# Kernel optimization log

Hardware: AMD Instinct MI355X
Metric: run time of the kernel (lower is better)

The kernel has to match this reference:

```python
import jax, jax.numpy as jnp
import numpy as np

N = 100000   # nodes
E = 1600000  # edges
R = 5        # num relations = num_edge_types + 2
H = 64       # hidden_dim
K = 10000    # absorbed nodes (<= MAX_NODES PE table)
NT = 11      # num_node_types + 1
NB = 2       # num_bases


def setup_inputs() -> dict:
    key = jax.random.key(0)
    ks = jax.random.split(key, 20)
    x = jax.random.randint(ks[0], (N,), 0, NT, dtype=jnp.int32)
    edge_index = jax.random.randint(ks[1], (2, E), 0, N, dtype=jnp.int32)
    edge_type = jax.random.randint(ks[2], (E,), 0, R, dtype=jnp.int32)
    node_order = jnp.arange(K, dtype=jnp.int32)
    emb = jax.random.normal(ks[3], (NT, H), dtype=jnp.float32) * 0.1
    inp = {"x": x, "edge_index": edge_index, "edge_type": edge_type,
           "node_order": node_order, "emb": emb}
    dims = [(H, H), (H, H), (H, 1)]
    i = 4
    for l, (din, dout) in enumerate(dims):
        inp[f"bases{l}"] = jax.random.normal(ks[i], (NB, din, dout), dtype=jnp.float32) / np.sqrt(din); i += 1
        inp[f"comp{l}"] = jax.random.normal(ks[i], (R, NB), dtype=jnp.float32) * 0.5; i += 1
        inp[f"root{l}"] = jax.random.normal(ks[i], (din, dout), dtype=jnp.float32) / np.sqrt(din); i += 1
        inp[f"bias{l}"] = jnp.zeros((dout,), dtype=jnp.float32)
    return inp


def rgcn_conv(h, src, dst, etype, bases, comp, root, bias):
    # Basis decomposition: W_r = sum_b comp[r,b] * bases[b]   -> [R, in, out]
    W = jnp.einsum('rb,bio->rio', comp, bases)
    # Transform every node by every relation weight (small R), then gather per edge.
    xW = jnp.einsum('ni,rio->nro', h, W)            # [N, R, out]
    msg = xW[src, etype]                            # [E, out]
    # Per-relation MEAN aggregation (PyG RGCNConv default): normalize each edge
    # by the count of edges with the same (dst, relation).
    seg = dst * R + etype                           # [E]
    cnt = jax.ops.segment_sum(jnp.ones((E,), h.dtype), seg, num_segments=N * R)
    norm = 1.0 / jnp.maximum(cnt[seg], 1.0)         # [E]
    agg = jax.ops.segment_sum(msg * norm[:, None], dst, num_segments=N)  # [N, out]
    return agg + h @ root + bias


def reference(x, edge_index, edge_type, node_order, emb,
              bases0, comp0, root0, bias0,
              bases1, comp1, root1, bias1,
              bases2, comp2, root2, bias2):
    h = emb[x]                                      # [N, H]
    # Positional encoding with out_channels=1: pe[t, 0] = sin((t+1) * 1.0),
    # broadcast-added across the hidden dim of each absorbed node.
    pe = jnp.sin(jnp.arange(1, K + 1, dtype=jnp.float32))[:, None]  # [K, 1]
    h = h.at[node_order].add(jnp.broadcast_to(pe, (K, H)))
    src, dst = edge_index[0], edge_index[1]
    h = rgcn_conv(h, src, dst, edge_type, bases0, comp0, root0, bias0)
    h = rgcn_conv(h, src, dst, edge_type, bases1, comp1, root1, bias1)
    h = rgcn_conv(h, src, dst, edge_type, bases2, comp2, root2, bias2)  # [N, 1]
    absorbed = jnp.zeros((N,), bool).at[node_order].set(True)
    unmasked = (~absorbed).astype(h.dtype)[:, None]  # [N, 1]
    eh = jnp.exp(h)
    denom = jnp.sum(eh * unmasked, axis=0)           # sum over unmasked rows
    return (eh / denom) * unmasked                   # absorbed rows zeroed
```

## Files before the change

kernel.cpp:

```cpp
#include <hip/hip_runtime.h>
#include <hip/hip_fp16.h>
#include <math.h>

#define NN 100000
#define NE 1600000
#define RR 5
#define HH 64
#define KK 10000
#define NBB 2
#define NBK 391
#define EPB 6250
#define BSLOT 4608
#define MPITCH 136

typedef _Float16 f16x8 __attribute__((ext_vector_type(8)));
typedef float f32x4 __attribute__((ext_vector_type(4)));

__global__ void k_init_h(const int* __restrict__ x, const float4* __restrict__ emb4,
                         unsigned short* __restrict__ hH, int* __restrict__ bcur,
                         int* __restrict__ absorbed, float* __restrict__ denom) {
    int idx = blockIdx.x * blockDim.x + threadIdx.x;
    if (idx >= NN * 16) return;
    int n = idx >> 4;
    int q = idx & 15;
    float4 v = emb4[x[n] * 16 + q];
    __half2 lo = __floats2half2_rn(v.x, v.y);
    __half2 hi = __floats2half2_rn(v.z, v.w);
    *(uint2*)&hH[(size_t)n * HH + q * 4] = make_uint2(*(unsigned*)&lo, *(unsigned*)&hi);
    if (idx < NBK) bcur[idx] = 0;
    if (idx == NBK) denom[0] = 0.f;
    if (idx < NN) absorbed[idx] = 0;
}

__global__ void k_pe(const int* __restrict__ order, unsigned short* __restrict__ hH,
                     int* __restrict__ absorbed) {
    int idx = blockIdx.x * blockDim.x + threadIdx.x;
    if (idx >= KK * 16) return;
    int t = idx >> 4;
    int q = idx & 15;
    int node = order[t];
    float v = (float)sin((double)(t + 1));
    uint2 u = *(uint2*)&hH[(size_t)node * HH + q * 4];
    float2 lo = __half22float2(*(__half2*)&u.x);
    float2 hi = __half22float2(*(__half2*)&u.y);
    __half2 nlo = __floats2half2_rn(lo.x + v, lo.y + v);
    __half2 nhi = __floats2half2_rn(hi.x + v, hi.y + v);
    *(uint2*)&hH[(size_t)node * HH + q * 4] = make_uint2(*(unsigned*)&nlo, *(unsigned*)&nhi);
    if (q == 0) absorbed[node] = 1;
}

__global__ void k_bplace(const int* __restrict__ src, const int* __restrict__ dst,
                         const int* __restrict__ et, int* __restrict__ bcur,
                         unsigned int* __restrict__ ebuf) {
    __shared__ int hist[NBK];
    __shared__ int lbase[NBK];
    __shared__ int lcur[NBK];
    int tid = threadIdx.x;
    for (int i = tid; i < NBK; i += 256) { hist[i] = 0; lcur[i] = 0; }
    __syncthreads();
    int e0 = blockIdx.x * EPB;
    int e1 = e0 + EPB < NE ? e0 + EPB : NE;
    for (int e = e0 + tid; e < e1; e += 256)
        atomicAdd(&hist[dst[e] >> 8], 1);
    __syncthreads();
    for (int i = tid; i < NBK; i += 256)
        if (hist[i]) lbase[i] = i * BSLOT + atomicAdd(&bcur[i], hist[i]);
    __syncthreads();
    for (int e = e0 + tid; e < e1; e += 256) {
        int d = dst[e];
        int b = d >> 8;
        int r = atomicAdd(&lcur[b], 1);
        int idx = lbase[b] + r;
        if (idx < (b + 1) * BSLOT)
            ebuf[idx] = ((unsigned)(d & 255) << 20) | ((unsigned)src[e] << 3) | (unsigned)et[e];
    }
}

__launch_bounds__(256)
__global__ void k_bsort(const unsigned int* __restrict__ ebuf, const int* __restrict__ bcur,
                        unsigned int* __restrict__ epair, int2* __restrict__ rowse,
                        float* __restrict__ norm5g) {
    __shared__ unsigned int el[BSLOT];
    __shared__ int cnt5[256 * RR];
    __shared__ int dcur[256];
    __shared__ int s[256];
    int tid = threadIdx.x;
    int b = blockIdx.x;
    int base = b * BSLOT;
    int sz = bcur[b];
    if (sz > BSLOT) sz = BSLOT;

    for (int i = tid; i < sz; i += 256) el[i] = ebuf[base + i];
    for (int i = tid; i < 256 * RR; i += 256) cnt5[i] = 0;
    __syncthreads();
    for (int i = tid; i < sz; i += 256) {
        unsigned int e = el[i];
        atomicAdd(&cnt5[(e >> 20) * RR + (e & 7)], 1);
    }
    __syncthreads();
    int deg = 0;
#pragma unroll
    for (int r = 0; r < RR; r++) deg += cnt5[tid * RR + r];
    s[tid] = deg;
    dcur[tid] = 0;
    __syncthreads();
#pragma unroll
    for (int off = 1; off < 256; off <<= 1) {
        int t = (tid >= off) ? s[tid - off] : 0;
        __syncthreads();
        s[tid] += t;
        __syncthreads();
    }
    int rs = s[tid] - deg;
    int d = b * 256 + tid;
    if (d < NN) {
        rowse[d] = make_int2(base + rs, base + rs + deg);
#pragma unroll
        for (int r = 0; r < RR; r++) {
            int c = cnt5[tid * RR + r];
            norm5g[(size_t)d * RR + r] = 1.0f / (float)(c > 1 ? c : 1);
        }
    }
    __syncthreads();
    for (int i = tid; i < sz; i += 256) {
        unsigned int e = el[i];
        int d8 = e >> 20;
        int rk = atomicAdd(&dcur[d8], 1);
        int pos = base + (s[d8] - (cnt5[d8 * RR + 0] + cnt5[d8 * RR + 1] + cnt5[d8 * RR + 2]
                                   + cnt5[d8 * RR + 3] + cnt5[d8 * RR + 4])) + rk;
        unsigned int cnt = (unsigned)cnt5[d8 * RR + (e & 7)];
        epair[pos] = (cnt << 23) | (e & 0xFFFFFu);
    }
}

__global__ void k_makeWt(const float* __restrict__ b0, const float* __restrict__ r0,
                         const float* __restrict__ b1, const float* __restrict__ r1,
                         unsigned short* __restrict__ Wt) {
    int idx = blockIdx.x * 256 + threadIdx.x;
    if (idx >= 2 * 64 * 192) return;
    int layer = idx / (64 * 192);
    int rem = idx - layer * 64 * 192;
    int o = rem / 192, k = rem - o * 192;
    const float* bases = layer ? b1 : b0;
    const float* root  = layer ? r1 : r0;
    float w = (k < 64)  ? bases[(size_t)k * HH + o]
            : (k < 128) ? bases[(size_t)HH * HH + (size_t)(k - 64) * HH + o]
                        : root[(size_t)(k - 128) * HH + o];
    __half hv = __float2half_rn(w);
    Wt[idx] = *(unsigned short*)&hv;
}

template <int DO2>
__launch_bounds__(256)
__global__ void k_layer(const int2* __restrict__ rowse, const unsigned int* __restrict__ epair,
                        const float* __restrict__ norm5g, const float* __restrict__ comp,
                        const unsigned short* __restrict__ hH, const unsigned short* __restrict__ Wt,
                        const float* __restrict__ bias, unsigned short* __restrict__ outH,
                        const float* __restrict__ bases2, const float* __restrict__ comp2,
                        const float* __restrict__ root2, const float* __restrict__ bias2,
                        float* __restrict__ xW2, float* __restrict__ h2) {
    __shared__ float2 lut[8];
    __shared__ float2 wlutS[64][8];
    __shared__ _Float16 mixs[64][MPITCH];
    __shared__ float sW2[6 * HH];
    int tid = threadIdx.x;
    int wave = tid >> 6;
    int lane = tid & 63;
    if (tid < 8) {
        int r = tid < RR ? tid : 0;
        lut[tid] = make_float2(comp[r * NBB + 0], comp[r * NBB + 1]);
    }
    if (DO2) {
        for (int i2 = tid; i2 < 6 * HH; i2 += 256) {
            int c = i2 >> 6, k = i2 & 63;
            sW2[i2] = (c < RR) ? (comp2[c * NBB + 0] * bases2[k] + comp2[c * NBB + 1] * bases2[HH + k])
                               : root2[k];
        }
    }
    __syncthreads();

    int n0 = blockIdx.x * 64;
    int g  = lane >> 3;
    int dq = lane & 7;

    for (int i = 0; i < 2; ++i) {
        int row = wave * 16 + i * 8 + g;
        int node = n0 + row;
        float m0[8] = {}, m1[8] = {};
        int beg = 0, end = 0;
        if (node < NN) { int2 se = rowse[node]; beg = se.x; end = se.y; }
        float nv = (dq < RR && node < NN) ? norm5g[(size_t)node * RR + dq] : 0.f;
        float2 cw = (dq < RR) ? make_float2(lut[dq].x * nv, lut[dq].y * nv)
                              : make_float2(0.f, 0.f);
        wlutS[row][dq] = cw;

        unsigned int p[8];
#pragma unroll
        for (int u = 0; u < 8; ++u) p[u] = (beg + u < end) ? epair[beg + u] : 5u;
        for (int j = beg; j < end; j += 8) {
            unsigned int q[8];
#pragma unroll
            for (int u = 0; u < 8; ++u)
                q[u] = (j + 8 + u < end) ? epair[j + 8 + u] : 5u;
            uint4 ua[8];
#pragma unroll
            for (int u = 0; u < 8; ++u)
                ua[u] = *(const uint4*)&hH[(size_t)((p[u] >> 3) & 0x1FFFFu) * HH + dq * 8];
#pragma unroll
            for (int u = 0; u < 8; ++u) {
                float2 cc = wlutS[row][p[u] & 7];
                float a0 = cc.x, a1 = cc.y;
                float2 f;
                f = __half22float2(*(__half2*)&ua[u].x);
                m0[0] += a0 * f.x; m0[1] += a0 * f.y; m1[0] += a1 * f.x; m1[1] += a1 * f.y;
                f = __half22float2(*(__half2*)&ua[u].y);
                m0[2] += a0 * f.x; m0[3] += a0 * f.y; m1[2] += a1 * f.x; m1[3] += a1 * f.y;
                f = __half22float2(*(__half2*)&ua[u].z);
                m0[4] += a0 * f.x; m0[5] += a0 * f.y; m1[4] += a1 * f.x; m1[5] += a1 * f.y;
                f = __half22float2(*(__half2*)&ua[u].w);
                m0[6] += a0 * f.x; m0[7] += a0 * f.y; m1[6] += a1 * f.x; m1[7] += a1 * f.y;
            }
#pragma unroll
            for (int u = 0; u < 8; ++u) p[u] = q[u];
        }
        __half2 a01 = __floats2half2_rn(m0[0], m0[1]);
        __half2 a23 = __floats2half2_rn(m0[2], m0[3]);
        __half2 a45 = __floats2half2_rn(m0[4], m0[5]);
        __half2 a67 = __floats2half2_rn(m0[6], m0[7]);
        *(uint4*)&mixs[row][dq * 8] =
            make_uint4(*(unsigned*)&a01, *(unsigned*)&a23, *(unsigned*)&a45, *(unsigned*)&a67);
        __half2 b01 = __floats2half2_rn(m1[0], m1[1]);
        __half2 b23 = __floats2half2_rn(m1[2], m1[3]);
        __half2 b45 = __floats2half2_rn(m1[4], m1[5]);
        __half2 b67 = __floats2half2_rn(m1[6], m1[7]);
        *(uint4*)&mixs[row][64 + dq * 8] =
            make_uint4(*(unsigned*)&b01, *(unsigned*)&b23, *(unsigned*)&b45, *(unsigned*)&b67);
    }

    int lm = lane & 15;
    int lk = (lane >> 4) * 8;
    int rowA = wave * 16 + lm;
    int nodeA = n0 + rowA;
    int nodeClamp = nodeA < NN ? nodeA : NN - 1;

    f32x4 acc0 = {}, acc1 = {}, acc2 = {}, acc3 = {};
#pragma unroll
    for (int ks = 0; ks < 6; ++ks) {
        f16x8 a;
        if (ks < 4) a = *(const f16x8*)&mixs[rowA][ks * 32 + lk];
        else        a = *(const f16x8*)&hH[(size_t)nodeClamp * HH + (ks - 4) * 32 + lk];
        f16x8 b0 = *(const f16x8*)&Wt[(size_t)(0 * 16 + lm) * 192 + ks * 32 + lk];
        f16x8 b1 = *(const f16x8*)&Wt[(size_t)(1 * 16 + lm) * 192 + ks * 32 + lk];
        f16x8 b2 = *(const f16x8*)&Wt[(size_t)(2 * 16 + lm) * 192 + ks * 32 + lk];
        f16x8 b3 = *(const f16x8*)&Wt[(size_t)(3 * 16 + lm) * 192 + ks * 32 + lk];
        acc0 = __builtin_amdgcn_mfma_f32_16x16x32_f16(a, b0, acc0, 0, 0, 0);
        acc1 = __builtin_amdgcn_mfma_f32_16x16x32_f16(a, b1, acc1, 0, 0, 0);
        acc2 = __builtin_amdgcn_mfma_f32_16x16x32_f16(a, b2, acc2, 0, 0, 0);
        acc3 = __builtin_amdgcn_mfma_f32_16x16x32_f16(a, b3, acc3, 0, 0, 0);
    }

    float bv0 = bias[0 * 16 + lm];
    float bv1 = bias[1 * 16 + lm];
    float bv2 = bias[2 * 16 + lm];
    float bv3 = bias[3 * 16 + lm];

    int nrow = n0 + wave * 16 + (lane >> 4) * 4;
#pragma unroll
    for (int j = 0; j < 4; ++j) {
        int node = nrow + j;
        float v0 = acc0[j] + bv0;
        float v1 = acc1[j] + bv1;
        float v2 = acc2[j] + bv2;
        float v3 = acc3[j] + bv3;
        if (node < NN) {
            __half h0 = __float2half_rn(v0), h1 = __float2half_rn(v1);
            __half h2v = __float2half_rn(v2), h3 = __float2half_rn(v3);
            outH[(size_t)node * HH +  0 + lm] = *(unsigned short*)&h0;
            outH[(size_t)node * HH + 16 + lm] = *(unsigned short*)&h1;
            outH[(size_t)node * HH + 32 + lm] = *(unsigned short*)&h2v;
            outH[(size_t)node * HH + 48 + lm] = *(unsigned short*)&h3;
        }
        if (DO2) {
            float p0 = v0 * sW2[0 * HH + lm] + v1 * sW2[0 * HH + 16 + lm]
                     + v2 * sW2[0 * HH + 32 + lm] + v3 * sW2[0 * HH + 48 + lm];
            float p1 = v0 * sW2[1 * HH + lm] + v1 * sW2[1 * HH + 16 + lm]
                     + v2 * sW2[1 * HH + 32 + lm] + v3 * sW2[1 * HH + 48 + lm];
            float p2 = v0 * sW2[2 * HH + lm] + v1 * sW2[2 * HH + 16 + lm]
                     + v2 * sW2[2 * HH + 32 + lm] + v3 * sW2[2 * HH + 48 + lm];
            float p3 = v0 * sW2[3 * HH + lm] + v1 * sW2[3 * HH + 16 + lm]
                     + v2 * sW2[3 * HH + 32 + lm] + v3 * sW2[3 * HH + 48 + lm];
            float p4 = v0 * sW2[4 * HH + lm] + v1 * sW2[4 * HH + 16 + lm]
                     + v2 * sW2[4 * HH + 32 + lm] + v3 * sW2[4 * HH + 48 + lm];
            float p5 = v0 * sW2[5 * HH + lm] + v1 * sW2[5 * HH + 16 + lm]
                     + v2 * sW2[5 * HH + 32 + lm] + v3 * sW2[5 * HH + 48 + lm];
#pragma unroll
            for (int off = 1; off < 16; off <<= 1) {
                p0 += __shfl_xor(p0, off); p1 += __shfl_xor(p1, off);
                p2 += __shfl_xor(p2, off); p3 += __shfl_xor(p3, off);
                p4 += __shfl_xor(p4, off); p5 += __shfl_xor(p5, off);
            }
            if (lm == 0 && node < NN) {
                xW2[(size_t)node * RR + 0] = p0;
                xW2[(size_t)node * RR + 1] = p1;
                xW2[(size_t)node * RR + 2] = p2;
                xW2[(size_t)node * RR + 3] = p3;
                xW2[(size_t)node * RR + 4] = p4;
                h2[node] = p5 + bias2[0];
            }
        }
    }
}

__global__ void k_gather2(const int2* __restrict__ rowse, const unsigned int* __restrict__ epair,
                          const float* __restrict__ xW2, float* __restrict__ h2,
                          const int* __restrict__ absorbed, float* __restrict__ denom) {
    __shared__ float sdata[256];
    int tid = threadIdx.x;
    int n = blockIdx.x * blockDim.x + tid;
    float local = 0.f;
    if (n < NN) {
        int2 se = rowse[n];
        float acc = h2[n];
        for (int j = se.x; j < se.y; ++j) {
            unsigned int e = epair[j];
            int c = e >> 23;
            float nv = 1.0f / (float)(c > 1 ? c : 1);
            acc += nv * xW2[(size_t)((e >> 3) & 0x1FFFFu) * RR + (e & 7)];
        }
        h2[n] = acc;
        if (!absorbed[n]) local = expf(acc);
    }
    sdata[tid] = local;
    __syncthreads();
    for (int s = 128; s > 0; s >>= 1) {
        if (tid < s) sdata[tid] += sdata[tid + s];
        __syncthreads();
    }
    if (tid == 0) atomicAdd(denom, sdata[0]);
}

__global__ void k_final(const float* __restrict__ h2, const int* __restrict__ absorbed,
                        const float* __restrict__ denom, float* __restrict__ out) {
    int n = blockIdx.x * blockDim.x + threadIdx.x;
    if (n >= NN) return;
    out[n] = absorbed[n] ? 0.f : expf(h2[n]) / denom[0];
}

extern "C" void kernel_launch(void* const* d_in, const int* in_sizes, int n_in,
                              void* d_out, int out_size, void* d_ws, size_t ws_size,
                              hipStream_t stream) {
    const int* x     = (const int*)d_in[0];
    const int* ei    = (const int*)d_in[1];
    const int* et    = (const int*)d_in[2];
    const int* order = (const int*)d_in[3];
    const float* emb = (const float*)d_in[4];
    const float* bases[3] = {(const float*)d_in[5], (const float*)d_in[9],  (const float*)d_in[13]};
    const float* comp[3]  = {(const float*)d_in[6], (const float*)d_in[10], (const float*)d_in[14]};
    const float* root[3]  = {(const float*)d_in[7], (const float*)d_in[11], (const float*)d_in[15]};
    const float* bias[3]  = {(const float*)d_in[8], (const float*)d_in[12], (const float*)d_in[16]};
    const int* srcp = ei;
    const int* dstp = ei + NE;

    char* w = (char*)d_ws;
    size_t off = 0;
    auto alloc = [&](size_t bytes) -> void* {
        void* p = w + off;
        off = (off + bytes + 255) & ~(size_t)255;
        return p;
    };
    unsigned short* hHa = (unsigned short*)alloc((size_t)NN * HH * 2);
    unsigned short* hHb = (unsigned short*)alloc((size_t)NN * HH * 2);
    float* xW2      = (float*)alloc((size_t)NN * RR * 4);
    float* h2       = (float*)alloc((size_t)NN * 4);
    int*   absorbed = (int*)alloc((size_t)NN * 4);
    int2*  rowse    = (int2*)alloc((size_t)NN * 8);
    float* norm5g   = (float*)alloc((size_t)NN * RR * 4);
    int*   bcur     = (int*)alloc((size_t)NBK * 4);
    unsigned int* ebuf  = (unsigned int*)alloc((size_t)NBK * BSLOT * 4);
    unsigned int* epair = (unsigned int*)alloc((size_t)NBK * BSLOT * 4);
    unsigned short* Wt  = (unsigned short*)alloc((size_t)2 * 64 * 192 * 2);
    float* denom    = (float*)alloc(256);

    k_init_h<<<(NN * 16 + 255) / 256, 256, 0, stream>>>(x, (const float4*)emb, hHa,
                                                        bcur, absorbed, denom);
    k_pe<<<(KK * 16 + 255) / 256, 256, 0, stream>>>(order, hHa, absorbed);

    k_makeWt<<<96, 256, 0, stream>>>(bases[0], root[0], bases[1], root[1], Wt);
    k_bplace<<<256, 256, 0, stream>>>(srcp, dstp, et, bcur, ebuf);
    k_bsort<<<NBK, 256, 0, stream>>>(ebuf, bcur, epair, rowse, norm5g);

    int glayer = (NN + 63) / 64;

    k_layer<0><<<glayer, 256, 0, stream>>>(rowse, epair, norm5g, comp[0], hHa, Wt, bias[0], hHb,
                                           nullptr, nullptr, nullptr, nullptr, nullptr, nullptr);
    k_layer<1><<<glayer, 256, 0, stream>>>(rowse, epair, norm5g, comp[1], hHb,
                                           Wt + (size_t)64 * 192, bias[1], hHa,
                                           bases[2], comp[2], root[2], bias[2], xW2, h2);

    k_gather2<<<(NN + 255) / 256, 256, 0, stream>>>(rowse, epair, xW2, h2, absorbed, denom);
    k_final<<<(NN + 255) / 256, 256, 0, stream>>>(h2, absorbed, denom, (float*)d_out);
}
```

Measured before the change: 175.7 us.

## Fuse weight prep into init kernel, add nontemporal gathers and MFMA priority

Folds the fp16 weight-transposition kernel into the embedding init kernel by adding extra threads, removing one launch. The random neighbour-row gathers in the layer and final gather kernels switch to nontemporal loads to reduce cache pollution, and the MFMA section is wrapped in raised wave priority. Nontemporal loads on the gathered features may cost reuse, since many edges share source rows that could otherwise hit in cache.

```diff
diff --git a/kernel.cpp b/kernel.cpp
--- a/kernel.cpp
+++ b/kernel.cpp
@@ -12,24 +12,42 @@
 #define EPB 6250
 #define BSLOT 4608
 #define MPITCH 136
+#define NWT (2 * 64 * 192)
 
 typedef _Float16 f16x8 __attribute__((ext_vector_type(8)));
 typedef float f32x4 __attribute__((ext_vector_type(4)));
+typedef unsigned int u32x4 __attribute__((ext_vector_type(4)));
 
 __global__ void k_init_h(const int* __restrict__ x, const float4* __restrict__ emb4,
                          unsigned short* __restrict__ hH, int* __restrict__ bcur,
-                         int* __restrict__ absorbed, float* __restrict__ denom) {
+                         int* __restrict__ absorbed, float* __restrict__ denom,
+                         const float* __restrict__ b0, const float* __restrict__ r0,
+                         const float* __restrict__ b1, const float* __restrict__ r1,
+                         unsigned short* __restrict__ Wt) {
     int idx = blockIdx.x * blockDim.x + threadIdx.x;
-    if (idx >= NN * 16) return;
-    int n = idx >> 4;
-    int q = idx & 15;
-    float4 v = emb4[x[n] * 16 + q];
-    __half2 lo = __floats2half2_rn(v.x, v.y);
-    __half2 hi = __floats2half2_rn(v.z, v.w);
-    *(uint2*)&hH[(size_t)n * HH + q * 4] = make_uint2(*(unsigned*)&lo, *(unsigned*)&hi);
-    if (idx < NBK) bcur[idx] = 0;
-    if (idx == NBK) denom[0] = 0.f;
-    if (idx < NN) absorbed[idx] = 0;
+    if (idx < NN * 16) {
+        int n = idx >> 4;
+        int q = idx & 15;
+        float4 v = emb4[x[n] * 16 + q];
+        __half2 lo = __floats2half2_rn(v.x, v.y);
+        __half2 hi = __floats2half2_rn(v.z, v.w);
+        *(uint2*)&hH[(size_t)n * HH + q * 4] = make_uint2(*(unsigned*)&lo, *(unsigned*)&hi);
+        if (idx < NBK) bcur[idx] = 0;
+        if (idx == NBK) denom[0] = 0.f;
+        if (idx < NN) absorbed[idx] = 0;
+    } else if (idx < NN * 16 + NWT) {
+        int widx = idx - NN * 16;
+        int layer = widx / (64 * 192);
+        int rem = widx - layer * 64 * 192;
+        int o = rem / 192, k = rem - o * 192;
+        const float* bases = layer ? b1 : b0;
+        const float* root  = layer ? r1 : r0;
+        float w = (k < 64)  ? bases[(size_t)k * HH + o]
+                : (k < 128) ? bases[(size_t)HH * HH + (size_t)(k - 64) * HH + o]
+                            : root[(size_t)(k - 128) * HH + o];
+        __half hv = __float2half_rn(w);
+        Wt[widx] = *(unsigned short*)&hv;
+    }
 }
 
 __global__ void k_pe(const int* __restrict__ order, unsigned short* __restrict__ hH,
@@ -131,23 +149,6 @@
         unsigned int cnt = (unsigned)cnt5[d8 * RR + (e & 7)];
         epair[pos] = (cnt << 23) | (e & 0xFFFFFu);
     }
-}
-
-__global__ void k_makeWt(const float* __restrict__ b0, const float* __restrict__ r0,
-                         const float* __restrict__ b1, const float* __restrict__ r1,
-                         unsigned short* __restrict__ Wt) {
-    int idx = blockIdx.x * 256 + threadIdx.x;
-    if (idx >= 2 * 64 * 192) return;
-    int layer = idx / (64 * 192);
-    int rem = idx - layer * 64 * 192;
-    int o = rem / 192, k = rem - o * 192;
-    const float* bases = layer ? b1 : b0;
-    const float* root  = layer ? r1 : r0;
-    float w = (k < 64)  ? bases[(size_t)k * HH + o]
-            : (k < 128) ? bases[(size_t)HH * HH + (size_t)(k - 64) * HH + o]
-                        : root[(size_t)(k - 128) * HH + o];
-    __half hv = __float2half_rn(w);
-    Wt[idx] = *(unsigned short*)&hv;
 }
 
 template <int DO2>
@@ -202,22 +203,24 @@
 #pragma unroll
             for (int u = 0; u < 8; ++u)
                 q[u] = (j + 8 + u < end) ? epair[j + 8 + u] : 5u;
-            uint4 ua[8];
+            u32x4 ua[8];
 #pragma unroll
             for (int u = 0; u < 8; ++u)
-                ua[u] = *(const uint4*)&hH[(size_t)((p[u] >> 3) & 0x1FFFFu) * HH + dq * 8];
+                ua[u] = __builtin_nontemporal_load(
+                    (const u32x4*)&hH[(size_t)((p[u] >> 3) & 0x1FFFFu) * HH + dq * 8]);
 #pragma unroll
             for (int u = 0; u < 8; ++u) {
                 float2 cc = wlutS[row][p[u] & 7];
                 float a0 = cc.x, a1 = cc.y;
+                unsigned w0 = ua[u][0], w1 = ua[u][1], w2 = ua[u][2], w3 = ua[u][3];
                 float2 f;
-                f = __half22float2(*(__half2*)&ua[u].x);
+                f = __half22float2(*(__half2*)&w0);
                 m0[0] += a0 * f.x; m0[1] += a0 * f.y; m1[0] += a1 * f.x; m1[1] += a1 * f.y;
-                f = __half22float2(*(__half2*)&ua[u].y);
+                f = __half22float2(*(__half2*)&w1);
                 m0[2] += a0 * f.x; m0[3] += a0 * f.y; m1[2] += a1 * f.x; m1[3] += a1 * f.y;
-                f = __half22float2(*(__half2*)&ua[u].z);
+                f = __half22float2(*(__half2*)&w2);
                 m0[4] += a0 * f.x; m0[5] += a0 * f.y; m1[4] += a1 * f.x; m1[5] += a1 * f.y;
-                f = __half22float2(*(__half2*)&ua[u].w);
+                f = __half22float2(*(__half2*)&w3);
                 m0[6] += a0 * f.x; m0[7] += a0 * f.y; m1[6] += a1 * f.x; m1[7] += a1 * f.y;
             }
 #pragma unroll
@@ -244,11 +247,13 @@
     int nodeClamp = nodeA < NN ? nodeA : NN - 1;
 
     f32x4 acc0 = {}, acc1 = {}, acc2 = {}, acc3 = {};
+    __builtin_amdgcn_s_setprio(1);
 #pragma unroll
     for (int ks = 0; ks < 6; ++ks) {
         f16x8 a;
         if (ks < 4) a = *(const f16x8*)&mixs[rowA][ks * 32 + lk];
-        else        a = *(const f16x8*)&hH[(size_t)nodeClamp * HH + (ks - 4) * 32 + lk];
+        else        a = __builtin_nontemporal_load(
+                        (const f16x8*)&hH[(size_t)nodeClamp * HH + (ks - 4) * 32 + lk]);
         f16x8 b0 = *(const f16x8*)&Wt[(size_t)(0 * 16 + lm) * 192 + ks * 32 + lk];
         f16x8 b1 = *(const f16x8*)&Wt[(size_t)(1 * 16 + lm) * 192 + ks * 32 + lk];
         f16x8 b2 = *(const f16x8*)&Wt[(size_t)(2 * 16 + lm) * 192 + ks * 32 + lk];
@@ -258,6 +263,7 @@
         acc2 = __builtin_amdgcn_mfma_f32_16x16x32_f16(a, b2, acc2, 0, 0, 0);
         acc3 = __builtin_amdgcn_mfma_f32_16x16x32_f16(a, b3, acc3, 0, 0, 0);
     }
+    __builtin_amdgcn_s_setprio(0);
 
     float bv0 = bias[0 * 16 + lm];
     float bv1 = bias[1 * 16 + lm];
@@ -325,7 +331,7 @@
             unsigned int e = epair[j];
             int c = e >> 23;
             float nv = 1.0f / (float)(c > 1 ? c : 1);
-            acc += nv * xW2[(size_t)((e >> 3) & 0x1FFFFu) * RR + (e & 7)];
+            acc += nv * __builtin_nontemporal_load(&xW2[(size_t)((e >> 3) & 0x1FFFFu) * RR + (e & 7)]);
         }
         h2[n] = acc;
         if (!absorbed[n]) local = expf(acc);
@@ -378,14 +384,14 @@
     int*   bcur     = (int*)alloc((size_t)NBK * 4);
     unsigned int* ebuf  = (unsigned int*)alloc((size_t)NBK * BSLOT * 4);
     unsigned int* epair = (unsigned int*)alloc((size_t)NBK * BSLOT * 4);
-    unsigned short* Wt  = (unsigned short*)alloc((size_t)2 * 64 * 192 * 2);
+    unsigned short* Wt  = (unsigned short*)alloc((size_t)NWT * 2);
     float* denom    = (float*)alloc(256);
 
-    k_init_h<<<(NN * 16 + 255) / 256, 256, 0, stream>>>(x, (const float4*)emb, hHa,
-                                                        bcur, absorbed, denom);
+    k_init_h<<<(NN * 16 + NWT + 255) / 256, 256, 0, stream>>>(x, (const float4*)emb, hHa,
+                                                              bcur, absorbed, denom,
+                                                              bases[0], root[0], bases[1], root[1], Wt);
     k_pe<<<(KK * 16 + 255) / 256, 256, 0, stream>>>(order, hHa, absorbed);
 
-    k_makeWt<<<96, 256, 0, stream>>>(bases[0], root[0], bases[1], root[1], Wt);
     k_bplace<<<256, 256, 0, stream>>>(srcp, dstp, et, bcur, ebuf);
     k_bsort<<<NBK, 256, 0, stream>>>(ebuf, bcur, epair, rowse, norm5g);
 
```

Result: slower. 214.6 us (+22.1%).
